# Kernel tuning notes

Measured on AMD Instinct MI355X. Metric: run time of the kernel, lower is better.

The kernel has to match this reference:

```python
import jax, jax.numpy as jnp
import numpy as np

N = 10000  # num_users + num_posts


def gcn_conv(x, edge_index, W, b):
    """PyG-style GCNConv: out = D^-1/2 (A+I) D^-1/2 (x W) + b."""
    h = x @ W  # [N, d]
    src, dst = edge_index[0], edge_index[1]
    loop = jnp.arange(N, dtype=src.dtype)
    src = jnp.concatenate([src, loop])
    dst = jnp.concatenate([dst, loop])
    ones = jnp.ones(src.shape[0], dtype=h.dtype)
    deg = jax.ops.segment_sum(ones, dst, num_segments=N)  # in-degree incl. self-loop
    dinv = jnp.where(deg > 0, jax.lax.rsqrt(deg), 0.0)
    norm = dinv[src] * dinv[dst]  # [E+N]
    msg = h[src] * norm[:, None]  # gather + scale
    out = jax.ops.segment_sum(msg, dst, num_segments=N)  # scatter-add
    return out + b


def setup_inputs() -> dict:
    key = jax.random.key(0)
    k1, k2, k3, k4 = jax.random.split(key, 4)
    E = 320000
    H = 64
    x = jax.random.normal(k1, (N, N), dtype=jnp.float32)
    edge_index = jax.random.randint(k2, (2, E), 0, N, dtype=jnp.int64)
    W1 = jax.random.normal(k3, (N, H), dtype=jnp.float32) / np.sqrt(N)
    b1 = jnp.zeros((H,), dtype=jnp.float32)
    W2 = jax.random.normal(k4, (H, H), dtype=jnp.float32) / np.sqrt(H)
    b2 = jnp.zeros((H,), dtype=jnp.float32)
    return {"x": x, "edge_index": edge_index, "W1": W1, "b1": b1, "W2": W2, "b2": b2}


def reference(x, edge_index, W1, b1, W2, b2):
    h = gcn_conv(x, edge_index, W1, b1)
    h = jax.nn.relu(h)
    return gcn_conv(h, edge_index, W2, b2)
```

## Files before the change

kernel.cpp:

```cpp
#include <hip/hip_runtime.h>
#include <hip/hip_bf16.h>

#define NND 10000
#define HD 64
#define KPAD 10112
#define ROWS 64
#define RBLK 157
#define KSTEP 128
#define KHEAD 5632
#define CAP 96
#define ABYTES 32768
#define BBYTES 16384
#define BUFB (ABYTES + BBYTES)
#define GRID 512

typedef __attribute__((ext_vector_type(8))) short bf16x8;
typedef __attribute__((ext_vector_type(4))) float f32x4;

__device__ __forceinline__ short f2bf(float f) {
    unsigned u = __builtin_bit_cast(unsigned, f);
    u += 0x7FFFu + ((u >> 16) & 1u);
    return (short)(u >> 16);
}

__device__ __forceinline__ void gload16(const void* gp, void* lp) {
    __builtin_amdgcn_global_load_lds(
        (const __attribute__((address_space(1))) unsigned int*)gp,
        (__attribute__((address_space(3))) unsigned int*)lp, 16, 0, 0);
}

__device__ __forceinline__ void gload16nt(const void* gp, void* lp) {
    __builtin_amdgcn_global_load_lds(
        (const __attribute__((address_space(1))) unsigned int*)gp,
        (__attribute__((address_space(3))) unsigned int*)lp, 16, 0, 2);
}

__global__ __launch_bounds__(256) void prep2_kernel(const float* __restrict__ W1,
        int* __restrict__ cnt, float* __restrict__ h, short* __restrict__ w1t) {
    __shared__ float tile[64][65];
    const int t = threadIdx.x;
    const int k0 = blockIdx.x * 64;
    #pragma unroll
    for (int i = 0; i < 16; ++i) {
        int r = i * 4 + (t >> 6);
        int c = t & 63;
        int k = k0 + r;
        tile[r][c] = (k < NND) ? W1[(size_t)k * HD + c] : 0.f;
    }
    __syncthreads();
    #pragma unroll
    for (int i = 0; i < 16; ++i) {
        int c = i * 4 + (t >> 6);
        int k = t & 63;
        if (k0 + k < KPAD)
            w1t[(size_t)c * KPAD + k0 + k] = f2bf(tile[k][c]);
    }
    int tid = blockIdx.x * 256 + t;
    if (tid < NND) cnt[tid] = 0;
    f32x4* h4 = (f32x4*)h;
    f32x4 z = {0.f, 0.f, 0.f, 0.f};
    #pragma unroll
    for (int i = 0; i < 4; ++i) {
        int idx = tid + i * 40448;
        if (idx < NND * HD / 4) h4[idx] = z;
    }
}

__global__ __launch_bounds__(512, 1) void csrgemm1_kernel(const float* __restrict__ x,
        const short* __restrict__ w1t, float* __restrict__ h,
        const int* __restrict__ ei, int* __restrict__ cnt, int* __restrict__ csr, int E) {
    {
        const int stride = GRID * 512;
        for (int e = blockIdx.x * 512 + threadIdx.x; e < E; e += stride) {
            int s = ei[e], d = ei[E + e];
            int pos = atomicAdd(&cnt[d], 1);
            if (pos < CAP) csr[d * CAP + pos] = s;
        }
    }
    asm volatile("s_waitcnt vmcnt(0)" ::: "memory");
    __shared__ f32x4 smem4[3 * BUFB / 16];
    char* smem = (char*)smem4;
    const int l = threadIdx.x & 63;
    const int w = threadIdx.x >> 6;
    int g, c, nch;
    {
        const int b = blockIdx.x;
        if (b < 164) { g = b >> 2; c = b & 3; nch = 4; }
        else { int bb = b - 164; int q = bb / 3; g = 41 + q; c = bb - q * 3; nch = 3; }
    }
    const int r0 = g * ROWS;
    int kstart, nsteps;
    if (nch == 4) { kstart = c * 20 * KSTEP; nsteps = (c == 3) ? 19 : 20; }
    else          { kstart = c * 27 * KSTEP; nsteps = (c == 2) ? 25 : 27; }

    const int wr = (w & 3) * 16;
    const int wc = (w >> 2) * 32;
    const int akg = l >> 4;
    const int l15 = l & 15;
    const int l7 = l & 7;

    f32x4 acc[2];
    acc[0] = f32x4{0.f, 0.f, 0.f, 0.f};
    acc[1] = f32x4{0.f, 0.f, 0.f, 0.f};

    union AFU { bf16x8 v; __hip_bfloat162 p[4]; };

    auto stage = [&](int buf, int k0) {
        char* sb = smem + buf * BUFB;
        const bool cached = (k0 < KHEAD);
        #pragma unroll
        for (int i = 0; i < 4; ++i) {
            int row = w * 8 + i * 2 + (l >> 5);
            int rg = r0 + row; if (rg >= NND) rg = 0;
            int pl = ((l & 31) >> 1) ^ (row & 7);
            const char* gp = (const char*)x + (size_t)rg * (NND * 4)
                             + (size_t)k0 * 4 + pl * 32 + (l & 1) * 16;
            if (k0 + pl * 8 + (l & 1) * 4 + 3 >= NND)
                gp = (const char*)x;
            if (cached) gload16(gp, sb + w * 4096 + i * 1024);
            else        gload16nt(gp, sb + w * 4096 + i * 1024);
        }
        #pragma unroll
        for (int j = 0; j < 2; ++j) {
            int col = w * 8 + j * 4 + (l >> 4);
            int cl = (l & 15) ^ (col & 7);
            const char* gp = (const char*)w1t + (size_t)col * (KPAD * 2)
                             + (size_t)k0 * 2 + cl * 16;
            gload16(gp, sb + ABYTES + w * 2048 + j * 1024);
        }
    };

    stage(0, kstart);
    if (nsteps > 1) stage(1, kstart + KSTEP);
    for (int t = 0; t < nsteps; ++t) {
        if (t + 1 < nsteps) asm volatile("s_waitcnt vmcnt(6)" ::: "memory");
        else                asm volatile("s_waitcnt vmcnt(0)" ::: "memory");
        __builtin_amdgcn_s_barrier();
        if (t + 2 < nsteps) stage((t + 2) % 3, kstart + (t + 2) * KSTEP);
        const char* sb = smem + (t % 3) * BUFB;
        #pragma unroll
        for (int ks = 0; ks < 4; ++ks) {
            int cp = (ks * 4 + akg) ^ l7;
            int arow = wr + l15;
            const char* ap = sb + arow * 512 + cp * 32;
            f32x4 a0 = *(const f32x4*)ap;
            f32x4 a1 = *(const f32x4*)(ap + 16);
            AFU af;
            af.p[0] = __float22bfloat162_rn(float2{a0[0], a0[1]});
            af.p[1] = __float22bfloat162_rn(float2{a0[2], a0[3]});
            af.p[2] = __float22bfloat162_rn(float2{a1[0], a1[1]});
            af.p[3] = __float22bfloat162_rn(float2{a1[2], a1[3]});
            #pragma unroll
            for (int cg = 0; cg < 2; ++cg) {
                int col = wc + cg * 16 + l15;
                bf16x8 b = *(const bf16x8*)(sb + ABYTES + col * 256 + cp * 16);
                acc[cg] = __builtin_amdgcn_mfma_f32_16x16x32_bf16(af.v, b, acc[cg], 0, 0, 0);
            }
        }
    }
    {
        const int crow = r0 + wr + akg * 4;
        #pragma unroll
        for (int cg = 0; cg < 2; ++cg) {
            const int ccol = wc + cg * 16 + l15;
            #pragma unroll
            for (int j = 0; j < 4; ++j) {
                int row = crow + j;
                if (row < NND)
                    unsafeAtomicAdd(&h[(size_t)row * HD + ccol], acc[cg][j]);
            }
        }
    }
}

__global__ __launch_bounds__(256) void scale_h_kernel(float* __restrict__ h,
        const int* __restrict__ cnt) {
    const int wave = threadIdx.x >> 6, lane = threadIdx.x & 63;
    const int r = blockIdx.x * 4 + wave;
    if (r >= NND) return;
    const float dd = rsqrtf((float)(min(cnt[r], CAP) + 1));
    h[(size_t)r * HD + lane] *= dd;
}

__global__ __launch_bounds__(256) void agg1g2_kernel(const float* __restrict__ h,
        const int* __restrict__ csr, const int* __restrict__ cnt,
        const float* __restrict__ b1, const float* __restrict__ W2,
        float* __restrict__ h2) {
    __shared__ float w2s[HD * HD];
    __shared__ float rowbuf[4][HD];
    for (int i = threadIdx.x; i < HD * HD; i += 256) w2s[i] = W2[i];
    const int wave = threadIdx.x >> 6, lane = threadIdx.x & 63;
    const int d = blockIdx.x * 4 + wave;
    const int n = min(cnt[d], CAP);
    const float dd = rsqrtf((float)(n + 1));
    float t0 = h[(size_t)d * HD + lane];
    float t1 = 0.f, t2 = 0.f, t3 = 0.f, t4 = 0.f, t5 = 0.f, t6 = 0.f, t7 = 0.f;
    const int* row = csr + d * CAP;
    int j = 0;
    for (; j + 16 <= n; j += 16) {
        int a0 = row[j],    a1 = row[j+1],  a2 = row[j+2],  a3 = row[j+3];
        int a4 = row[j+4],  a5 = row[j+5],  a6 = row[j+6],  a7 = row[j+7];
        int a8 = row[j+8],  a9 = row[j+9],  aa = row[j+10], ab = row[j+11];
        int ac = row[j+12], ad = row[j+13], ae = row[j+14], af = row[j+15];
        t0 += h[(size_t)a0 * HD + lane];  t1 += h[(size_t)a1 * HD + lane];
        t2 += h[(size_t)a2 * HD + lane];  t3 += h[(size_t)a3 * HD + lane];
        t4 += h[(size_t)a4 * HD + lane];  t5 += h[(size_t)a5 * HD + lane];
        t6 += h[(size_t)a6 * HD + lane];  t7 += h[(size_t)a7 * HD + lane];
        t0 += h[(size_t)a8 * HD + lane];  t1 += h[(size_t)a9 * HD + lane];
        t2 += h[(size_t)aa * HD + lane];  t3 += h[(size_t)ab * HD + lane];
        t4 += h[(size_t)ac * HD + lane];  t5 += h[(size_t)ad * HD + lane];
        t6 += h[(size_t)ae * HD + lane];  t7 += h[(size_t)af * HD + lane];
    }
    for (; j + 8 <= n; j += 8) {
        int a0 = row[j],   a1 = row[j+1], a2 = row[j+2], a3 = row[j+3];
        int a4 = row[j+4], a5 = row[j+5], a6 = row[j+6], a7 = row[j+7];
        t0 += h[(size_t)a0 * HD + lane];  t1 += h[(size_t)a1 * HD + lane];
        t2 += h[(size_t)a2 * HD + lane];  t3 += h[(size_t)a3 * HD + lane];
        t4 += h[(size_t)a4 * HD + lane];  t5 += h[(size_t)a5 * HD + lane];
        t6 += h[(size_t)a6 * HD + lane];  t7 += h[(size_t)a7 * HD + lane];
    }
    for (; j < n; ++j) t0 += h[(size_t)row[j] * HD + lane];
    float sum = ((t0 + t1) + (t2 + t3)) + ((t4 + t5) + (t6 + t7));
    float acc = fmaf(sum, dd, b1[lane]);
    rowbuf[wave][lane] = fmaxf(acc, 0.f);
    __syncthreads();
    float s = 0.f;
    #pragma unroll
    for (int k = 0; k < HD; ++k)
        s = fmaf(rowbuf[wave][k], w2s[k * HD + lane], s);
    h2[(size_t)d * HD + lane] = s * dd;
}

__global__ __launch_bounds__(256) void agg2_kernel(const float* __restrict__ feat,
        const int* __restrict__ csr, const int* __restrict__ cnt,
        const float* __restrict__ bias, float* __restrict__ out) {
    const int wave = threadIdx.x >> 6, lane = threadIdx.x & 63;
    const int d = blockIdx.x * 4 + wave;
    const int n = min(cnt[d], CAP);
    const float dd = rsqrtf((float)(n + 1));
    float t0 = feat[(size_t)d * HD + lane];
    float t1 = 0.f, t2 = 0.f, t3 = 0.f, t4 = 0.f, t5 = 0.f, t6 = 0.f, t7 = 0.f;
    const int* row = csr + d * CAP;
    int j = 0;
    for (; j + 16 <= n; j += 16) {
        int a0 = row[j],    a1 = row[j+1],  a2 = row[j+2],  a3 = row[j+3];
        int a4 = row[j+4],  a5 = row[j+5],  a6 = row[j+6],  a7 = row[j+7];
        int a8 = row[j+8],  a9 = row[j+9],  aa = row[j+10], ab = row[j+11];
        int ac = row[j+12], ad = row[j+13], ae = row[j+14], af = row[j+15];
        t0 += feat[(size_t)a0 * HD + lane];  t1 += feat[(size_t)a1 * HD + lane];
        t2 += feat[(size_t)a2 * HD + lane];  t3 += feat[(size_t)a3 * HD + lane];
        t4 += feat[(size_t)a4 * HD + lane];  t5 += feat[(size_t)a5 * HD + lane];
        t6 += feat[(size_t)a6 * HD + lane];  t7 += feat[(size_t)a7 * HD + lane];
        t0 += feat[(size_t)a8 * HD + lane];  t1 += feat[(size_t)a9 * HD + lane];
        t2 += feat[(size_t)aa * HD + lane];  t3 += feat[(size_t)ab * HD + lane];
        t4 += feat[(size_t)ac * HD + lane];  t5 += feat[(size_t)ad * HD + lane];
        t6 += feat[(size_t)ae * HD + lane];  t7 += feat[(size_t)af * HD + lane];
    }
    for (; j + 8 <= n; j += 8) {
        int a0 = row[j],   a1 = row[j+1], a2 = row[j+2], a3 = row[j+3];
        int a4 = row[j+4], a5 = row[j+5], a6 = row[j+6], a7 = row[j+7];
        t0 += feat[(size_t)a0 * HD + lane];  t1 += feat[(size_t)a1 * HD + lane];
        t2 += feat[(size_t)a2 * HD + lane];  t3 += feat[(size_t)a3 * HD + lane];
        t4 += feat[(size_t)a4 * HD + lane];  t5 += feat[(size_t)a5 * HD + lane];
        t6 += feat[(size_t)a6 * HD + lane];  t7 += feat[(size_t)a7 * HD + lane];
    }
    for (; j < n; ++j) t0 += feat[(size_t)row[j] * HD + lane];
    float sum = ((t0 + t1) + (t2 + t3)) + ((t4 + t5) + (t6 + t7));
    out[(size_t)d * HD + lane] = fmaf(sum, dd, bias[lane]);
}

extern "C" void kernel_launch(void* const* d_in, const int* in_sizes, int n_in,
                              void* d_out, int out_size, void* d_ws, size_t ws_size,
                              hipStream_t stream) {
    const float* x  = (const float*)d_in[0];
    const int*   ei = (const int*)d_in[1];
    const float* W1 = (const float*)d_in[2];
    const float* b1 = (const float*)d_in[3];
    const float* W2 = (const float*)d_in[4];
    const float* b2 = (const float*)d_in[5];
    float* out = (float*)d_out;
    const int E = in_sizes[1] / 2;

    char* ws = (char*)d_ws;
    int*   cnt  = (int*)(ws);
    float* h    = (float*)(ws + 40000);
    float* h2   = (float*)(ws + 2600000);
    short* w1t  = (short*)(ws + 5160000);
    int*   csr  = (int*)(ws + 6454336);

    prep2_kernel<<<158, 256, 0, stream>>>(W1, cnt, h, w1t);
    csrgemm1_kernel<<<GRID, 512, 0, stream>>>(x, w1t, h, ei, cnt, csr, E);
    scale_h_kernel<<<2500, 256, 0, stream>>>(h, cnt);
    agg1g2_kernel<<<2500, 256, 0, stream>>>(h, csr, cnt, b1, W2, h2);
    agg2_kernel<<<2500, 256, 0, stream>>>(h2, csr, cnt, b2, out);
}
```

Baseline: 128.3 us.

## Enlarge GEMM row tile to 112 with 14 waves, double-buffer LDS

The first-layer GEMM kernel now uses 112-row tiles with 896 threads (14 waves) per block. This cuts how many times the W1 column tiles are re-read across row groups, and the split-K partitioning is rebalanced into 6 or 5 chunks. To fit the larger A tile in LDS, the pipeline drops from triple to double buffering. That adds an extra barrier per K step and leaves less prefetch depth to hide the streaming loads of x.

```diff
diff --git a/kernel.cpp b/kernel.cpp
--- a/kernel.cpp
+++ b/kernel.cpp
@@ -4,15 +4,15 @@
 #define NND 10000
 #define HD 64
 #define KPAD 10112
-#define ROWS 64
-#define RBLK 157
+#define MROWS 112
 #define KSTEP 128
 #define KHEAD 5632
 #define CAP 96
-#define ABYTES 32768
+#define ABYTES 57344
 #define BBYTES 16384
 #define BUFB (ABYTES + BBYTES)
 #define GRID 512
+#define TPB 896
 
 typedef __attribute__((ext_vector_type(8))) short bf16x8;
 typedef __attribute__((ext_vector_type(4))) float f32x4;
@@ -66,35 +66,40 @@
     }
 }
 
-__global__ __launch_bounds__(512, 1) void csrgemm1_kernel(const float* __restrict__ x,
+__global__ __launch_bounds__(TPB, 1) void csrgemm1_kernel(const float* __restrict__ x,
         const short* __restrict__ w1t, float* __restrict__ h,
         const int* __restrict__ ei, int* __restrict__ cnt, int* __restrict__ csr, int E) {
     {
-        const int stride = GRID * 512;
-        for (int e = blockIdx.x * 512 + threadIdx.x; e < E; e += stride) {
+        const int stride = GRID * TPB;
+        for (int e = blockIdx.x * TPB + threadIdx.x; e < E; e += stride) {
             int s = ei[e], d = ei[E + e];
             int pos = atomicAdd(&cnt[d], 1);
             if (pos < CAP) csr[d * CAP + pos] = s;
         }
     }
     asm volatile("s_waitcnt vmcnt(0)" ::: "memory");
-    __shared__ f32x4 smem4[3 * BUFB / 16];
+    __shared__ f32x4 smem4[2 * BUFB / 16];
     char* smem = (char*)smem4;
     const int l = threadIdx.x & 63;
     const int w = threadIdx.x >> 6;
     int g, c, nch;
     {
         const int b = blockIdx.x;
-        if (b < 164) { g = b >> 2; c = b & 3; nch = 4; }
-        else { int bb = b - 164; int q = bb / 3; g = 41 + q; c = bb - q * 3; nch = 3; }
-    }
-    const int r0 = g * ROWS;
+        if (b < 372) { g = b / 6; c = b % 6; nch = 6; }
+        else { int bb = b - 372; g = 62 + bb / 5; c = bb % 5; nch = 5; }
+    }
+    const int r0 = g * MROWS;
     int kstart, nsteps;
-    if (nch == 4) { kstart = c * 20 * KSTEP; nsteps = (c == 3) ? 19 : 20; }
-    else          { kstart = c * 27 * KSTEP; nsteps = (c == 2) ? 25 : 27; }
-
-    const int wr = (w & 3) * 16;
-    const int wc = (w >> 2) * 32;
+    if (nch == 6) {
+        kstart = (c == 0) ? 0 : (14 + 13 * (c - 1)) * KSTEP;
+        nsteps = (c == 0) ? 14 : 13;
+    } else {
+        kstart = (c < 4) ? c * 16 * KSTEP : 64 * KSTEP;
+        nsteps = (c == 4) ? 15 : 16;
+    }
+
+    const int wr = (w % 7) * 16;
+    const int wc = (w / 7) * 32;
     const int akg = l >> 4;
     const int l15 = l & 15;
     const int l7 = l & 7;
@@ -120,24 +125,34 @@
             if (cached) gload16(gp, sb + w * 4096 + i * 1024);
             else        gload16nt(gp, sb + w * 4096 + i * 1024);
         }
-        #pragma unroll
-        for (int j = 0; j < 2; ++j) {
-            int col = w * 8 + j * 4 + (l >> 4);
+        {
+            int col = w * 4 + (l >> 4);
             int cl = (l & 15) ^ (col & 7);
             const char* gp = (const char*)w1t + (size_t)col * (KPAD * 2)
                              + (size_t)k0 * 2 + cl * 16;
-            gload16(gp, sb + ABYTES + w * 2048 + j * 1024);
+            gload16(gp, sb + ABYTES + w * 1024);
+        }
+        if (w < 2) {
+            int u = 14 + w;
+            int col = u * 4 + (l >> 4);
+            int cl = (l & 15) ^ (col & 7);
+            const char* gp = (const char*)w1t + (size_t)col * (KPAD * 2)
+                             + (size_t)k0 * 2 + cl * 16;
+            gload16(gp, sb + ABYTES + u * 1024);
         }
     };
 
     stage(0, kstart);
-    if (nsteps > 1) stage(1, kstart + KSTEP);
     for (int t = 0; t < nsteps; ++t) {
-        if (t + 1 < nsteps) asm volatile("s_waitcnt vmcnt(6)" ::: "memory");
-        else                asm volatile("s_waitcnt vmcnt(0)" ::: "memory");
+        if (t + 1 < nsteps) {
+            stage((t + 1) & 1, kstart + (t + 1) * KSTEP);
+            if (w < 2) asm volatile("s_waitcnt vmcnt(6)" ::: "memory");
+            else       asm volatile("s_waitcnt vmcnt(5)" ::: "memory");
+        } else {
+            asm volatile("s_waitcnt vmcnt(0)" ::: "memory");
+        }
         __builtin_amdgcn_s_barrier();
-        if (t + 2 < nsteps) stage((t + 2) % 3, kstart + (t + 2) * KSTEP);
-        const char* sb = smem + (t % 3) * BUFB;
+        const char* sb = smem + (t & 1) * BUFB;
         #pragma unroll
         for (int ks = 0; ks < 4; ++ks) {
             int cp = (ks * 4 + akg) ^ l7;
@@ -157,6 +172,7 @@
                 acc[cg] = __builtin_amdgcn_mfma_f32_16x16x32_bf16(af.v, b, acc[cg], 0, 0, 0);
             }
         }
+        __builtin_amdgcn_s_barrier();
     }
     {
         const int crow = r0 + wr + akg * 4;
@@ -289,7 +305,7 @@
     int*   csr  = (int*)(ws + 6454336);
 
     prep2_kernel<<<158, 256, 0, stream>>>(W1, cnt, h, w1t);
-    csrgemm1_kernel<<<GRID, 512, 0, stream>>>(x, w1t, h, ei, cnt, csr, E);
+    csrgemm1_kernel<<<GRID, TPB, 0, stream>>>(x, w1t, h, ei, cnt, csr, E);
     scale_h_kernel<<<2500, 256, 0, stream>>>(h, cnt);
     agg1g2_kernel<<<2500, 256, 0, stream>>>(h, csr, cnt, b1, W2, h2);
     agg2_kernel<<<2500, 256, 0, stream>>>(h2, csr, cnt, b2, out);
```

Result: slower. 137.2 us (+6.9%).
